# Kernel optimization log

Measured on AMD Instinct MI355X. Metric: run time of the kernel, lower is better.

## Reference

```python
import jax, jax.numpy as jnp
import numpy as np

HEADS = 8
NEG_SLOPE = 0.2
N_REL = 3
N_NODES = 10000
N_EDGES = 160000
OBS = 32
ACT = 8
N_GRAPHS = 16
HC = HEADS * OBS  # 256 = heads * out_channels (dim=1)


def _rgat_layer(x, w, q, k, e, we, b, src, dst, etype, eattr):
    """PyG RGATConv, additive-self-attention, across-relation, dim=1, concat=True, eval mode."""
    N = x.shape[0]
    # relation-specific transform for every node, then per-edge gather (avoids [E,in,out] bmm)
    xw = jnp.einsum('ni,rio->nro', x, w)              # [N, R, H*C]
    outi = xw[dst, etype]                              # [E, H*C] target features
    outj = xw[src, etype]                              # [E, H*C] source features
    alpha = outi @ q + outj @ k + (eattr @ we) @ e     # [E, H]
    alpha = jax.nn.leaky_relu(alpha, NEG_SLOPE)
    # segment softmax over destination neighborhoods (PyG softmax: detached max, +1e-16)
    amax = jax.lax.stop_gradient(jax.ops.segment_max(alpha, dst, num_segments=N))
    amax = jnp.where(jnp.isfinite(amax), amax, 0.0)
    ex = jnp.exp(alpha - amax[dst])
    denom = jax.ops.segment_sum(ex, dst, num_segments=N)
    attn = ex / (denom[dst] + 1e-16)                   # [E, H]
    E_ = outj.shape[0]
    msg = attn[:, :, None] * outj.reshape(E_, HEADS, -1)  # [E, H, C]
    agg = jax.ops.segment_sum(msg, dst, num_segments=N)   # [N, H, C]
    return agg.reshape(N, -1) + b                          # concat heads + bias


def setup_inputs() -> dict:
    key = jax.random.key(0)
    ks = jax.random.split(key, 32)
    s = 0.05
    inp = {
        'x': jax.random.normal(ks[0], (N_NODES, OBS), jnp.float32),
        'edge_index': jax.random.randint(ks[1], (2, N_EDGES), 0, N_NODES),
        'edge_type': jax.random.randint(ks[2], (N_EDGES,), 0, N_REL),
        'edge_attr': jax.random.normal(ks[3], (N_EDGES, 1), jnp.float32),
        'batch': jnp.sort(jax.random.randint(ks[4], (N_NODES,), 0, N_GRAPHS)),
    }
    ins = [OBS, HC, HC]
    i = 5
    for l, cin in enumerate(ins, start=1):
        inp[f'w{l}'] = s * jax.random.normal(ks[i + 0], (N_REL, cin, HC), jnp.float32)
        inp[f'q{l}'] = s * jax.random.normal(ks[i + 1], (HC, HEADS), jnp.float32)
        inp[f'k{l}'] = s * jax.random.normal(ks[i + 2], (HC, HEADS), jnp.float32)
        inp[f'e{l}'] = s * jax.random.normal(ks[i + 3], (HC, HEADS), jnp.float32)
        inp[f'we{l}'] = s * jax.random.normal(ks[i + 4], (1, HC), jnp.float32)
        inp[f'b{l}'] = jnp.zeros((HC,), jnp.float32)
        i += 5
    inp['wlin'] = s * jax.random.normal(ks[i], (HC, ACT), jnp.float32)
    inp['blin'] = jnp.zeros((ACT,), jnp.float32)
    return inp


def reference(x, edge_index, edge_type, edge_attr, batch,
              w1, q1, k1, e1, we1, b1,
              w2, q2, k2, e2, we2, b2,
              w3, q3, k3, e3, we3, b3,
              wlin, blin):
    src, dst = edge_index[0], edge_index[1]
    h = jax.nn.relu(_rgat_layer(x, w1, q1, k1, e1, we1, b1, src, dst, edge_type, edge_attr))
    h = jax.nn.relu(_rgat_layer(h, w2, q2, k2, e2, we2, b2, src, dst, edge_type, edge_attr))
    h = jax.nn.relu(_rgat_layer(h, w3, q3, k3, e3, we3, b3, src, dst, edge_type, edge_attr))
    h = jnp.tanh(h @ wlin + blin)                        # [N, ACT]
    sums = jax.ops.segment_sum(h, batch, num_segments=N_GRAPHS)
    cnts = jax.ops.segment_sum(jnp.ones((h.shape[0], 1), h.dtype), batch, num_segments=N_GRAPHS)
    return sums / jnp.maximum(cnts, 1.0)                 # global_mean_pool -> [G, ACT]
```

## Files before the change

kernel.cpp:

```cpp
#include <hip/hip_runtime.h>
#include <math.h>

#define HEADS 8
#define HC 256
#define NREL 3
#define NEG 0.2f
#define MAXDEG 128
#define PCHUNK 8
#define NCT 17

typedef float vfloat4 __attribute__((ext_vector_type(4)));
typedef short b16x8 __attribute__((ext_vector_type(8)));
typedef float f32x4 __attribute__((ext_vector_type(4)));

__device__ __forceinline__ float warp32_reduce(float p) {
#pragma unroll
    for (int off = 16; off > 0; off >>= 1) p += __shfl_down(p, off, 32);
    return p;
}

__device__ __forceinline__ unsigned short f2bf(float f) {
    unsigned u = __float_as_uint(f);
    unsigned r = (u + 0x7FFFu + ((u >> 16) & 1u)) >> 16;
    return (unsigned short)r;
}
__device__ __forceinline__ float bf2f(unsigned short b) {
    return __uint_as_float(((unsigned)b) << 16);
}

__global__ void k_wprep(
    const float* __restrict__ W1, const float* __restrict__ Q1, const float* __restrict__ K1,
    const float* __restrict__ E1, const float* __restrict__ WE1,
    const float* __restrict__ W2, const float* __restrict__ Q2, const float* __restrict__ K2,
    const float* __restrict__ E2, const float* __restrict__ WE2,
    const float* __restrict__ W3, const float* __restrict__ Q3, const float* __restrict__ K3,
    const float* __restrict__ E3, const float* __restrict__ WE3,
    unsigned short* __restrict__ b1hi, unsigned short* __restrict__ b1lo,
    unsigned short* __restrict__ b2hi, unsigned short* __restrict__ b2lo,
    unsigned short* __restrict__ b3hi, unsigned short* __restrict__ b3lo,
    float* __restrict__ wee,
    const float* __restrict__ x, unsigned short* __restrict__ x1hi,
    unsigned short* __restrict__ x1lo,
    const int* __restrict__ ei, const int* __restrict__ et, const float* __restrict__ ea,
    int* __restrict__ fill, int* __restrict__ bpack, float* __restrict__ bae,
    int nnodes, int nedges, int nprep, int npacka) {
    int bi = blockIdx.x;
    int tid = threadIdx.x;
    if (bi >= nprep + npacka) {
        int e = (bi - nprep - npacka) * 256 + tid;
        if (e < nedges) {
            int dst = ei[nedges + e];
            int pos = atomicAdd(&fill[dst], 1);
            if (pos < MAXDEG) {
                bpack[dst * MAXDEG + pos] = (ei[e] << 2) | (et[e] & 3);
                bae[dst * MAXDEG + pos] = ea[e];
            }
        }
        return;
    }
    if (bi >= nprep) {
        int i = (bi - nprep) * 256 + tid;
        if (i < nnodes * 32) {
            int n = i >> 5, k = i & 31;
            float f = x[i];
            unsigned short h = f2bf(f);
            int ntile = n >> 4, m = n & 15;
            int q = (k >> 3) & 3, j = k & 7;
            size_t o = ((size_t)ntile * 64 + q * 16 + m) * 8 + j;
            x1hi[o] = h;
            x1lo[o] = f2bf(f - bf2f(h));
        }
        return;
    }
    const float *w, *qm, *km, *em, *wem;
    unsigned short *bhi, *blo;
    int K, layer, lbi;
    if (bi < NREL * 32) {
        layer = 0; lbi = bi; K = 32;
        w = W1; qm = Q1; km = K1; em = E1; wem = WE1; bhi = b1hi; blo = b1lo;
    } else if (bi < NREL * 32 + NREL * HC) {
        layer = 1; lbi = bi - NREL * 32; K = HC;
        w = W2; qm = Q2; km = K2; em = E2; wem = WE2; bhi = b2hi; blo = b2lo;
    } else {
        layer = 2; lbi = bi - NREL * 32 - NREL * HC; K = HC;
        w = W3; qm = Q3; km = K3; em = E3; wem = WE3; bhi = b3hi; blo = b3lo;
    }
    int r = lbi / K, i = lbi - r * K;
    int KB = K / 32;
    int kb = i >> 5, qq = (i >> 3) & 3, j = i & 7;
    {
        int c = tid;
        float f = w[(size_t)lbi * HC + c];
        unsigned short h = f2bf(f);
        int ct = c >> 4, mc = c & 15;
        size_t o = ((((size_t)r * NCT + ct) * KB + kb) * 64 + qq * 16 + mc) * 8 + j;
        bhi[o] = h;
        blo[o] = f2bf(f - bf2f(h));
    }
    int h = tid >> 5, lane = tid & 31;
    const float* wrow = w + (size_t)lbi * HC;
    size_t base = (((size_t)r * NCT + 16) * KB + kb) * 512 + j;
    float p = 0.f;
    for (int o = lane; o < HC; o += 32) p += wrow[o] * qm[o * HEADS + h];
    p = warp32_reduce(p);
    if (lane == 0) {
        size_t o = base + (size_t)(qq * 16 + h) * 8;
        unsigned short hh = f2bf(p);
        bhi[o] = hh;
        blo[o] = f2bf(p - bf2f(hh));
    }
    p = 0.f;
    for (int o = lane; o < HC; o += 32) p += wrow[o] * km[o * HEADS + h];
    p = warp32_reduce(p);
    if (lane == 0) {
        size_t o = base + (size_t)(qq * 16 + 8 + h) * 8;
        unsigned short hh = f2bf(p);
        bhi[o] = hh;
        blo[o] = f2bf(p - bf2f(hh));
    }
    if (lbi == 0 && tid < HEADS) {
        float s = 0.f;
        for (int o = 0; o < HC; o++) s += wem[o] * em[o * HEADS + tid];
        wee[layer * HEADS + tid] = s;
    }
}

template <int K, int NT>
__global__ __launch_bounds__(256) void k_mfma(const unsigned short* __restrict__ pahi,
                                              const unsigned short* __restrict__ palo,
                                              const unsigned short* __restrict__ pbhi,
                                              const unsigned short* __restrict__ pblo,
                                              float* __restrict__ xw,
                                              float* __restrict__ qdot,
                                              float* __restrict__ kdot,
                                              int nnodes, int ntiles) {
    constexpr int KB = K / 32;
    int ntg = blockIdx.x;
    int r = blockIdx.y;
    int t = threadIdx.x;
    int wv = t >> 6, lane = t & 63;
    int q = lane >> 4, m = lane & 15;
    f32x4 acc[5][NT] = {};
    for (int kb = 0; kb < KB; ++kb) {
        b16x8 ah[NT], al[NT];
#pragma unroll
        for (int ti = 0; ti < NT; ++ti) {
            int nt = ntg * NT + ti;
            if (nt >= ntiles) nt = ntiles - 1;
            size_t ao = (((size_t)nt * KB + kb) * 64 + lane) * 8;
            ah[ti] = *(const b16x8*)(pahi + ao);
            al[ti] = *(const b16x8*)(palo + ao);
        }
#pragma unroll
        for (int s = 0; s < 5; ++s) {
            int ct = wv + 4 * s;
            if (ct >= NCT) continue;
            size_t o = (((size_t)r * NCT + ct) * KB + kb) * 512 + (size_t)lane * 8;
            b16x8 vbh = *(const b16x8*)(pbhi + o);
            b16x8 vbl = *(const b16x8*)(pblo + o);
#pragma unroll
            for (int ti = 0; ti < NT; ++ti) {
                acc[s][ti] = __builtin_amdgcn_mfma_f32_16x16x32_bf16(ah[ti], vbh, acc[s][ti], 0, 0, 0);
                acc[s][ti] = __builtin_amdgcn_mfma_f32_16x16x32_bf16(al[ti], vbh, acc[s][ti], 0, 0, 0);
                acc[s][ti] = __builtin_amdgcn_mfma_f32_16x16x32_bf16(ah[ti], vbl, acc[s][ti], 0, 0, 0);
            }
        }
    }
#pragma unroll
    for (int ti = 0; ti < NT; ++ti) {
        int nt = ntg * NT + ti;
        if (nt >= ntiles) continue;
        int n0 = nt * 16;
#pragma unroll
        for (int s = 0; s < 5; ++s) {
            int ct = wv + 4 * s;
            if (ct >= NCT) continue;
            if (ct < 16) {
                int c = ct * 16 + m;
#pragma unroll
                for (int g = 0; g < 4; ++g) {
                    int n = n0 + q * 4 + g;
                    if (n < nnodes) xw[((size_t)n * NREL + r) * HC + c] = acc[s][ti][g];
                }
            } else {
#pragma unroll
                for (int g = 0; g < 4; ++g) {
                    int n = n0 + q * 4 + g;
                    if (n < nnodes) {
                        if (m < 8) qdot[n * 24 + r * 8 + m] = acc[s][ti][g];
                        else       kdot[n * 24 + r * 8 + (m - 8)] = acc[s][ti][g];
                    }
                }
            }
        }
    }
}

__global__ __launch_bounds__(256) void k_agg(const float* __restrict__ xw,
                      const float* __restrict__ qdot, const float* __restrict__ kdot,
                      const int* __restrict__ fill, const int* __restrict__ bpack,
                      const float* __restrict__ bae, const float* __restrict__ wee,
                      const float* __restrict__ bias, float* __restrict__ hout,
                      unsigned short* __restrict__ houthi, unsigned short* __restrict__ houtlo,
                      int nnodes) {
    __shared__ float salpha[4][MAXDEG * HEADS];
    __shared__ int spack[4][MAXDEG];
    int wv = threadIdx.x >> 6, lane = threadIdx.x & 63;
    int n = blockIdx.x * 4 + wv;
    if (n >= nnodes) return;
    int beg = n * MAXDEG;
    int deg = fill[n];
    if (deg > MAXDEG) deg = MAXDEG;
    float* sal = salpha[wv];
    int* spk = spack[wv];
    {
        int h = lane & 7;
        float weeh = wee[h];
        const float* qdn = qdot + n * 24;
        for (int base = 0; base < deg; base += 8) {
            int d = base + (lane >> 3);
            if (d < deg) {
                int pk = bpack[beg + d];
                float ae = bae[beg + d];
                int s = pk >> 2, t = pk & 3;
                if (h == 0) spk[d] = pk;
                float a = qdn[t * 8 + h] + kdot[s * 24 + t * 8 + h] + ae * weeh;
                sal[d * 8 + h] = (a > 0.f) ? a : NEG * a;
            }
        }
    }
    float sinv_h;
    {
        int h = lane & 7, c = lane >> 3;
        float m = -INFINITY;
        for (int d = c; d < deg; d += 8) m = fmaxf(m, sal[d * 8 + h]);
        m = fmaxf(m, __shfl_xor(m, 8, 64));
        m = fmaxf(m, __shfl_xor(m, 16, 64));
        m = fmaxf(m, __shfl_xor(m, 32, 64));
        float s = 0.f;
        for (int d = c; d < deg; d += 8) {
            float ex = expf(sal[d * 8 + h] - m);
            sal[d * 8 + h] = ex;
            s += ex;
        }
        s += __shfl_xor(s, 8, 64);
        s += __shfl_xor(s, 16, 64);
        s += __shfl_xor(s, 32, 64);
        sinv_h = 1.f / (s + 1e-16f);
    }
    float sinv_sel = __shfl(sinv_h, lane >> 3, 64);
    int hsel = lane >> 3;
    float4 acc4 = make_float4(0.f, 0.f, 0.f, 0.f);
    int d = 0;
    for (; d + 3 < deg; d += 4) {
        int pk0 = spk[d], pk1 = spk[d + 1], pk2 = spk[d + 2], pk3 = spk[d + 3];
        const float4* r0 = (const float4*)(xw + ((size_t)(pk0 >> 2) * NREL + (pk0 & 3)) * HC);
        const float4* r1 = (const float4*)(xw + ((size_t)(pk1 >> 2) * NREL + (pk1 & 3)) * HC);
        const float4* r2 = (const float4*)(xw + ((size_t)(pk2 >> 2) * NREL + (pk2 & 3)) * HC);
        const float4* r3 = (const float4*)(xw + ((size_t)(pk3 >> 2) * NREL + (pk3 & 3)) * HC);
        float4 v0 = r0[lane], v1 = r1[lane], v2 = r2[lane], v3 = r3[lane];
        float a0 = sal[d * 8 + hsel];
        float a1 = sal[(d + 1) * 8 + hsel];
        float a2 = sal[(d + 2) * 8 + hsel];
        float a3 = sal[(d + 3) * 8 + hsel];
        acc4.x += a0 * v0.x + a1 * v1.x + a2 * v2.x + a3 * v3.x;
        acc4.y += a0 * v0.y + a1 * v1.y + a2 * v2.y + a3 * v3.y;
        acc4.z += a0 * v0.z + a1 * v1.z + a2 * v2.z + a3 * v3.z;
        acc4.w += a0 * v0.w + a1 * v1.w + a2 * v2.w + a3 * v3.w;
    }
    for (; d < deg; ++d) {
        int pk = spk[d];
        const float4* r0 = (const float4*)(xw + ((size_t)(pk >> 2) * NREL + (pk & 3)) * HC);
        float4 v0 = r0[lane];
        float a0 = sal[d * 8 + hsel];
        acc4.x += a0 * v0.x;
        acc4.y += a0 * v0.y;
        acc4.z += a0 * v0.z;
        acc4.w += a0 * v0.w;
    }
    float4 bv = *(const float4*)(bias + lane * 4);
    float4 v;
    v.x = fmaxf(acc4.x * sinv_sel + bv.x, 0.f);
    v.y = fmaxf(acc4.y * sinv_sel + bv.y, 0.f);
    v.z = fmaxf(acc4.z * sinv_sel + bv.z, 0.f);
    v.w = fmaxf(acc4.w * sinv_sel + bv.w, 0.f);
    *(float4*)(hout + (size_t)n * HC + lane * 4) = v;
    int ntile = n >> 4, mm = n & 15;
    float vv[4] = {v.x, v.y, v.z, v.w};
#pragma unroll
    for (int i = 0; i < 4; ++i) {
        int c = lane * 4 + i;
        int kb = c >> 5, q = (c >> 3) & 3, j = c & 7;
        size_t o2 = ((((size_t)ntile * 8 + kb) * 64) + q * 16 + mm) * 8 + j;
        unsigned short hh = f2bf(vv[i]);
        houthi[o2] = hh;
        houtlo[o2] = f2bf(vv[i] - bf2f(hh));
    }
}

__global__ __launch_bounds__(256) void k_pool2(const float* __restrict__ h3,
                                               const float* __restrict__ wlin,
                                               const float* __restrict__ blin,
                                               const int* __restrict__ batch,
                                               float* __restrict__ partials,
                                               int* __restrict__ gcnt, int* __restrict__ ctr,
                                               float* __restrict__ out, int nnodes, int ngraph) {
    int g = blockIdx.x / PCHUNK, chunk = blockIdx.x % PCHUNK;
    __shared__ int sb[2];
    if (threadIdx.x < 2) {
        int target = g + threadIdx.x;
        int lo = 0, hi = nnodes;
        while (lo < hi) { int mid = (lo + hi) >> 1; if (batch[mid] < target) lo = mid + 1; else hi = mid; }
        sb[threadIdx.x] = lo;
    }
    __syncthreads();
    int beg = sb[0], end = sb[1];
    int t = threadIdx.x;
    int w = t >> 6, lane = t & 63;
    int h = lane & 7, grp = lane >> 3;
    float rw[32];
#pragma unroll
    for (int k = 0; k < 8; ++k)
#pragma unroll
        for (int j = 0; j < 4; ++j)
            rw[k * 4 + j] = wlin[(grp * 4 + j + 32 * k) * HEADS + h];
    float bl = blin[h];
    float acc = 0.f;
    int wg = chunk * 4 + w;
    for (int n = beg + wg; n < end; n += PCHUNK * 4) {
        const float* row = h3 + (size_t)n * HC;
        float dot = 0.f;
#pragma unroll
        for (int k = 0; k < 8; ++k) {
            float4 v = *(const float4*)&row[grp * 4 + 32 * k];
            dot += v.x * rw[k * 4] + v.y * rw[k * 4 + 1] + v.z * rw[k * 4 + 2] + v.w * rw[k * 4 + 3];
        }
        dot += __shfl_xor(dot, 8, 64);
        dot += __shfl_xor(dot, 16, 64);
        dot += __shfl_xor(dot, 32, 64);
        acc += tanhf(dot + bl);
    }
    __shared__ float sacc[4][HEADS];
    __shared__ float sred[HEADS];
    __shared__ int slast;
    if (lane < HEADS) sacc[w][h] = acc;
    __syncthreads();
    if (t < HEADS) sred[t] = sacc[0][t] + sacc[1][t] + sacc[2][t] + sacc[3][t];
    __syncthreads();
    if (t == 0) {
        for (int hh = 0; hh < HEADS; ++hh)
            partials[(size_t)blockIdx.x * HEADS + hh] = sred[hh];
        if (chunk == 0) gcnt[g] = end - beg;
        __threadfence();
        slast = (atomicAdd(ctr, 1) == (int)gridDim.x - 1);
    }
    __syncthreads();
    if (slast) {
        __threadfence();
        if (t < ngraph * HEADS) {
            int gg = t >> 3, hh = t & 7;
            float s = 0.f;
            for (int c = 0; c < PCHUNK; ++c)
                s += partials[(size_t)(gg * PCHUNK + c) * HEADS + hh];
            out[t] = s / fmaxf((float)gcnt[gg], 1.f);
        }
    }
}


extern "C" void kernel_launch(void* const* d_in, const int* in_sizes, int n_in,
                              void* d_out, int out_size, void* d_ws, size_t ws_size,
                              hipStream_t stream) {
    const float* x    = (const float*)d_in[0];
    const int*   ei   = (const int*)d_in[1];
    const int*   et   = (const int*)d_in[2];
    const float* ea   = (const float*)d_in[3];
    const int*   batch = (const int*)d_in[4];
    const float* W[3]  = {(const float*)d_in[5],  (const float*)d_in[11], (const float*)d_in[17]};
    const float* Q[3]  = {(const float*)d_in[6],  (const float*)d_in[12], (const float*)d_in[18]};
    const float* K[3]  = {(const float*)d_in[7],  (const float*)d_in[13], (const float*)d_in[19]};
    const float* Em[3] = {(const float*)d_in[8],  (const float*)d_in[14], (const float*)d_in[20]};
    const float* WE[3] = {(const float*)d_in[9],  (const float*)d_in[15], (const float*)d_in[21]};
    const float* B[3]  = {(const float*)d_in[10], (const float*)d_in[16], (const float*)d_in[22]};
    const float* wlin = (const float*)d_in[23];
    const float* blin = (const float*)d_in[24];

    int nnodes = in_sizes[0] / 32;
    int nedges = in_sizes[2];
    int ngraph = 16;
    int npad = (nnodes + 15) & ~15;
    int ntiles = npad / 16;

    char* ws = (char*)d_ws;
    size_t off = 0;
    auto alloc = [&](size_t bytes) -> void* {
        void* p = ws + off;
        off = (off + bytes + 255) & ~(size_t)255;
        return p;
    };
    int*   fill     = (int*)alloc((size_t)(nnodes + 64) * 4);
    int*   ctr      = fill + nnodes;
    int*   bpack    = (int*)alloc((size_t)nnodes * MAXDEG * 4);
    float* bae      = (float*)alloc((size_t)nnodes * MAXDEG * 4);
    float* xw       = (float*)alloc((size_t)npad * NREL * HC * 4);
    float* qdot     = (float*)alloc((size_t)npad * NREL * HEADS * 4);
    float* kdot     = (float*)alloc((size_t)npad * NREL * HEADS * 4);
    float* ha       = (float*)alloc((size_t)nnodes * HC * 4);
    float* hb       = (float*)alloc((size_t)nnodes * HC * 4);
    float* wee      = (float*)alloc((size_t)NREL * HEADS * 4);
    float* partials = (float*)alloc((size_t)ngraph * PCHUNK * HEADS * 4);
    int*   gcnt     = (int*)alloc((size_t)ngraph * 4);
    unsigned short* x1hi = (unsigned short*)alloc((size_t)npad * 32 * 2);
    unsigned short* x1lo = (unsigned short*)alloc((size_t)npad * 32 * 2);
    unsigned short* hahi = (unsigned short*)alloc((size_t)npad * HC * 2);
    unsigned short* halo = (unsigned short*)alloc((size_t)npad * HC * 2);
    unsigned short* hbhi = (unsigned short*)alloc((size_t)npad * HC * 2);
    unsigned short* hblo = (unsigned short*)alloc((size_t)npad * HC * 2);
    unsigned short* wt1hi = (unsigned short*)alloc((size_t)NREL * NCT * 1 * 512 * 2);
    unsigned short* wt1lo = (unsigned short*)alloc((size_t)NREL * NCT * 1 * 512 * 2);
    unsigned short* wt2hi = (unsigned short*)alloc((size_t)NREL * NCT * 8 * 512 * 2);
    unsigned short* wt2lo = (unsigned short*)alloc((size_t)NREL * NCT * 8 * 512 * 2);
    unsigned short* wt3hi = (unsigned short*)alloc((size_t)NREL * NCT * 8 * 512 * 2);
    unsigned short* wt3lo = (unsigned short*)alloc((size_t)NREL * NCT * 8 * 512 * 2);
    (void)ws_size; (void)n_in; (void)out_size;

    int nprep = NREL * 32 + 2 * NREL * HC;
    int npacka = (nnodes * 32 + 255) / 256;
    int nscat = (nedges + 255) / 256;

    hipMemsetAsync(fill, 0, (size_t)(nnodes + 64) * 4, stream);
    k_wprep<<<nprep + npacka + nscat, 256, 0, stream>>>(
        W[0], Q[0], K[0], Em[0], WE[0],
        W[1], Q[1], K[1], Em[1], WE[1],
        W[2], Q[2], K[2], Em[2], WE[2],
        wt1hi, wt1lo, wt2hi, wt2lo, wt3hi, wt3lo, wee,
        x, x1hi, x1lo,
        ei, et, ea, fill, bpack, bae,
        nnodes, nedges, nprep, npacka);

    dim3 gmfma1(ntiles, NREL);
    dim3 gmfma2((ntiles + 1) / 2, NREL);
    int gagg = (nnodes + 3) / 4;

    k_mfma<32, 1><<<gmfma1, 256, 0, stream>>>(x1hi, x1lo, wt1hi, wt1lo, xw, qdot, kdot, nnodes, ntiles);
    k_agg<<<gagg, 256, 0, stream>>>(xw, qdot, kdot, fill, bpack, bae, wee + 0, B[0], ha, hahi, halo, nnodes);

    k_mfma<HC, 2><<<gmfma2, 256, 0, stream>>>(hahi, halo, wt2hi, wt2lo, xw, qdot, kdot, nnodes, ntiles);
    k_agg<<<gagg, 256, 0, stream>>>(xw, qdot, kdot, fill, bpack, bae, wee + 8, B[1], hb, hbhi, hblo, nnodes);

    k_mfma<HC, 2><<<gmfma2, 256, 0, stream>>>(hbhi, hblo, wt3hi, wt3lo, xw, qdot, kdot, nnodes, ntiles);
    k_agg<<<gagg, 256, 0, stream>>>(xw, qdot, kdot, fill, bpack, bae, wee + 16, B[2], ha, hahi, halo, nnodes);

    k_pool2<<<ngraph * PCHUNK, 256, 0, stream>>>(ha, wlin, blin, batch, partials, gcnt, ctr,
                                                 (float*)d_out, nnodes, ngraph);
}
```

Measured before the change: 312.1 us.

## Pack edge buckets, vectorize weight split, skip unused layer outputs

Weight conversion into bf16 hi/lo MFMA tiles moves to dedicated blocks that write 8-element vectors instead of scattered 2-byte stores. Edge source/type and attribute are packed into one int2 bucket, so the aggregation reads one 8-byte load per edge instead of two arrays. The aggregation kernel skips the fp32 output for layers 1-2 and the bf16 split output for layer 3, cutting global writes. Layer 1 MFMA also switches to the 2-tile-per-block variant. The main cost is extra template instantiation and a larger prep grid.

```diff
diff --git a/kernel.cpp b/kernel.cpp
--- a/kernel.cpp
+++ b/kernel.cpp
@@ -12,6 +12,7 @@
 typedef float vfloat4 __attribute__((ext_vector_type(4)));
 typedef short b16x8 __attribute__((ext_vector_type(8)));
 typedef float f32x4 __attribute__((ext_vector_type(4)));
+typedef unsigned short u16x8 __attribute__((ext_vector_type(8)));
 
 __device__ __forceinline__ float warp32_reduce(float p) {
 #pragma unroll
@@ -42,19 +43,48 @@
     const float* __restrict__ x, unsigned short* __restrict__ x1hi,
     unsigned short* __restrict__ x1lo,
     const int* __restrict__ ei, const int* __restrict__ et, const float* __restrict__ ea,
-    int* __restrict__ fill, int* __restrict__ bpack, float* __restrict__ bae,
-    int nnodes, int nedges, int nprep, int npacka) {
+    int* __restrict__ fill, int2* __restrict__ bkt,
+    int nnodes, int nedges, int nwcv, int nprep, int npacka) {
     int bi = blockIdx.x;
     int tid = threadIdx.x;
+    if (bi < nwcv) {
+        const float* w;
+        unsigned short *bhi, *blo;
+        int K, r, kb;
+        if (bi < NREL) { w = W1; bhi = b1hi; blo = b1lo; K = 32; r = bi; kb = 0; }
+        else if (bi < NREL + NREL * 8) {
+            int idx = bi - NREL; w = W2; bhi = b2hi; blo = b2lo; K = HC; r = idx >> 3; kb = idx & 7;
+        } else {
+            int idx = bi - NREL - NREL * 8; w = W3; bhi = b3hi; blo = b3lo; K = HC; r = idx >> 3; kb = idx & 7;
+        }
+        int KB = K / 32;
+        int ct = tid >> 4, mc = tid & 15;
+        int c = ct * 16 + mc;
+#pragma unroll
+        for (int q = 0; q < 4; ++q) {
+            u16x8 hv, lv;
+#pragma unroll
+            for (int j = 0; j < 8; ++j) {
+                float f = w[(size_t)(r * K + kb * 32 + q * 8 + j) * HC + c];
+                unsigned short h = f2bf(f);
+                hv[j] = h;
+                lv[j] = f2bf(f - bf2f(h));
+            }
+            size_t base = ((((size_t)r * NCT + ct) * KB + kb) * 64 + q * 16 + mc) * 8;
+            *(u16x8*)(bhi + base) = hv;
+            *(u16x8*)(blo + base) = lv;
+        }
+        return;
+    }
+    bi -= nwcv;
     if (bi >= nprep + npacka) {
         int e = (bi - nprep - npacka) * 256 + tid;
         if (e < nedges) {
             int dst = ei[nedges + e];
             int pos = atomicAdd(&fill[dst], 1);
-            if (pos < MAXDEG) {
-                bpack[dst * MAXDEG + pos] = (ei[e] << 2) | (et[e] & 3);
-                bae[dst * MAXDEG + pos] = ea[e];
-            }
+            if (pos < MAXDEG)
+                bkt[dst * MAXDEG + pos] = make_int2((ei[e] << 2) | (et[e] & 3),
+                                                    __float_as_int(ea[e]));
         }
         return;
     }
@@ -88,15 +118,6 @@
     int r = lbi / K, i = lbi - r * K;
     int KB = K / 32;
     int kb = i >> 5, qq = (i >> 3) & 3, j = i & 7;
-    {
-        int c = tid;
-        float f = w[(size_t)lbi * HC + c];
-        unsigned short h = f2bf(f);
-        int ct = c >> 4, mc = c & 15;
-        size_t o = ((((size_t)r * NCT + ct) * KB + kb) * 64 + qq * 16 + mc) * 8 + j;
-        bhi[o] = h;
-        blo[o] = f2bf(f - bf2f(h));
-    }
     int h = tid >> 5, lane = tid & 31;
     const float* wrow = w + (size_t)lbi * HC;
     size_t base = (((size_t)r * NCT + 16) * KB + kb) * 512 + j;
@@ -198,8 +219,8 @@
 
 __global__ __launch_bounds__(256) void k_agg(const float* __restrict__ xw,
                       const float* __restrict__ qdot, const float* __restrict__ kdot,
-                      const int* __restrict__ fill, const int* __restrict__ bpack,
-                      const float* __restrict__ bae, const float* __restrict__ wee,
+                      const int* __restrict__ fill, const int2* __restrict__ bkt,
+                      const float* __restrict__ wee,
                       const float* __restrict__ bias, float* __restrict__ hout,
                       unsigned short* __restrict__ houthi, unsigned short* __restrict__ houtlo,
                       int nnodes) {
@@ -220,8 +241,9 @@
         for (int base = 0; base < deg; base += 8) {
             int d = base + (lane >> 3);
             if (d < deg) {
-                int pk = bpack[beg + d];
-                float ae = bae[beg + d];
+                int2 pa = bkt[beg + d];
+                int pk = pa.x;
+                float ae = __int_as_float(pa.y);
                 int s = pk >> 2, t = pk & 3;
                 if (h == 0) spk[d] = pk;
                 float a = qdn[t * 8 + h] + kdot[s * 24 + t * 8 + h] + ae * weeh;
@@ -284,17 +306,19 @@
     v.y = fmaxf(acc4.y * sinv_sel + bv.y, 0.f);
     v.z = fmaxf(acc4.z * sinv_sel + bv.z, 0.f);
     v.w = fmaxf(acc4.w * sinv_sel + bv.w, 0.f);
-    *(float4*)(hout + (size_t)n * HC + lane * 4) = v;
-    int ntile = n >> 4, mm = n & 15;
-    float vv[4] = {v.x, v.y, v.z, v.w};
-#pragma unroll
-    for (int i = 0; i < 4; ++i) {
-        int c = lane * 4 + i;
-        int kb = c >> 5, q = (c >> 3) & 3, j = c & 7;
-        size_t o2 = ((((size_t)ntile * 8 + kb) * 64) + q * 16 + mm) * 8 + j;
-        unsigned short hh = f2bf(vv[i]);
-        houthi[o2] = hh;
-        houtlo[o2] = f2bf(vv[i] - bf2f(hh));
+    if (hout) *(float4*)(hout + (size_t)n * HC + lane * 4) = v;
+    if (houthi) {
+        int ntile = n >> 4, mm = n & 15;
+        float vv[4] = {v.x, v.y, v.z, v.w};
+#pragma unroll
+        for (int i = 0; i < 4; ++i) {
+            int c = lane * 4 + i;
+            int kb = c >> 5, q = (c >> 3) & 3, j = c & 7;
+            size_t o2 = ((((size_t)ntile * 8 + kb) * 64) + q * 16 + mm) * 8 + j;
+            unsigned short hh = f2bf(vv[i]);
+            houthi[o2] = hh;
+            houtlo[o2] = f2bf(vv[i] - bf2f(hh));
+        }
     }
 }
 
@@ -400,13 +424,11 @@
     };
     int*   fill     = (int*)alloc((size_t)(nnodes + 64) * 4);
     int*   ctr      = fill + nnodes;
-    int*   bpack    = (int*)alloc((size_t)nnodes * MAXDEG * 4);
-    float* bae      = (float*)alloc((size_t)nnodes * MAXDEG * 4);
+    int2*  bkt      = (int2*)alloc((size_t)nnodes * MAXDEG * 8);
     float* xw       = (float*)alloc((size_t)npad * NREL * HC * 4);
     float* qdot     = (float*)alloc((size_t)npad * NREL * HEADS * 4);
     float* kdot     = (float*)alloc((size_t)npad * NREL * HEADS * 4);
     float* ha       = (float*)alloc((size_t)nnodes * HC * 4);
-    float* hb       = (float*)alloc((size_t)nnodes * HC * 4);
     float* wee      = (float*)alloc((size_t)NREL * HEADS * 4);
     float* partials = (float*)alloc((size_t)ngraph * PCHUNK * HEADS * 4);
     int*   gcnt     = (int*)alloc((size_t)ngraph * 4);
@@ -424,32 +446,35 @@
     unsigned short* wt3lo = (unsigned short*)alloc((size_t)NREL * NCT * 8 * 512 * 2);
     (void)ws_size; (void)n_in; (void)out_size;
 
+    int nwcv = NREL * (1 + 8 + 8);
     int nprep = NREL * 32 + 2 * NREL * HC;
     int npacka = (nnodes * 32 + 255) / 256;
     int nscat = (nedges + 255) / 256;
 
     hipMemsetAsync(fill, 0, (size_t)(nnodes + 64) * 4, stream);
-    k_wprep<<<nprep + npacka + nscat, 256, 0, stream>>>(
+    k_wprep<<<nwcv + nprep + npacka + nscat, 256, 0, stream>>>(
         W[0], Q[0], K[0], Em[0], WE[0],
         W[1], Q[1], K[1], Em[1], WE[1],
         W[2], Q[2], K[2], Em[2], WE[2],
         wt1hi, wt1lo, wt2hi, wt2lo, wt3hi, wt3lo, wee,
         x, x1hi, x1lo,
-        ei, et, ea, fill, bpack, bae,
-        nnodes, nedges, nprep, npacka);
-
-    dim3 gmfma1(ntiles, NREL);
-    dim3 gmfma2((ntiles + 1) / 2, NREL);
+        ei, et, ea, fill, bkt,
+        nnodes, nedges, nwcv, nprep, npacka);
+
+    dim3 gmfma((ntiles + 1) / 2, NREL);
     int gagg = (nnodes + 3) / 4;
 
-    k_mfma<32, 1><<<gmfma1, 256, 0, stream>>>(x1hi, x1lo, wt1hi, wt1lo, xw, qdot, kdot, nnodes, ntiles);
-    k_agg<<<gagg, 256, 0, stream>>>(xw, qdot, kdot, fill, bpack, bae, wee + 0, B[0], ha, hahi, halo, nnodes);
-
-    k_mfma<HC, 2><<<gmfma2, 256, 0, stream>>>(hahi, halo, wt2hi, wt2lo, xw, qdot, kdot, nnodes, ntiles);
-    k_agg<<<gagg, 256, 0, stream>>>(xw, qdot, kdot, fill, bpack, bae, wee + 8, B[1], hb, hbhi, hblo, nnodes);
-
-    k_mfma<HC, 2><<<gmfma2, 256, 0, stream>>>(hbhi, hblo, wt3hi, wt3lo, xw, qdot, kdot, nnodes, ntiles);
-    k_agg<<<gagg, 256, 0, stream>>>(xw, qdot, kdot, fill, bpack, bae, wee + 16, B[2], ha, hahi, halo, nnodes);
+    k_mfma<32, 2><<<gmfma, 256, 0, stream>>>(x1hi, x1lo, wt1hi, wt1lo, xw, qdot, kdot, nnodes, ntiles);
+    k_agg<<<gagg, 256, 0, stream>>>(xw, qdot, kdot, fill, bkt, wee + 0, B[0],
+                                    nullptr, hahi, halo, nnodes);
+
+    k_mfma<HC, 2><<<gmfma, 256, 0, stream>>>(hahi, halo, wt2hi, wt2lo, xw, qdot, kdot, nnodes, ntiles);
+    k_agg<<<gagg, 256, 0, stream>>>(xw, qdot, kdot, fill, bkt, wee + 8, B[1],
+                                    nullptr, hbhi, hblo, nnodes);
+
+    k_mfma<HC, 2><<<gmfma, 256, 0, stream>>>(hbhi, hblo, wt3hi, wt3lo, xw, qdot, kdot, nnodes, ntiles);
+    k_agg<<<gagg, 256, 0, stream>>>(xw, qdot, kdot, fill, bkt, wee + 16, B[2],
+                                    ha, nullptr, nullptr, nnodes);
 
     k_pool2<<<ngraph * PCHUNK, 256, 0, stream>>>(ha, wlin, blin, batch, partials, gcnt, ctr,
                                                  (float*)d_out, nnodes, ngraph);
```

Result: no change. 307.9 us (-1.3%).
